# Performance work log

Hardware: AMD Instinct MI355X
Metric: run time of the kernel (lower is better)

Reference implementation:

```python
import jax, jax.numpy as jnp
import numpy as np

TEMPERATURE = 0.5
EPS = 1e-8  # matches F.cosine_similarity eps clamp


def setup_inputs() -> dict:
    key = jax.random.key(0)
    k1, k2 = jax.random.split(key)
    logits = jax.random.normal(k1, (8192, 256), dtype=jnp.float32)
    label = jax.random.randint(k2, (8192,), 0, 10, dtype=jnp.int64)
    return {"logits": logits, "label": label}


def reference(logits, label):
    n = label.shape[0]
    # pairwise cosine similarity via normalize + GEMM (same math as the
    # broadcasted F.cosine_similarity, without the O(n^2 d) intermediate)
    norms = jnp.maximum(jnp.linalg.norm(logits, axis=1, keepdims=True), EPS)
    xn = logits / norms                       # [n, d]
    sim_matrix = xn @ xn.T                    # [n, n]

    eye = jnp.eye(n, dtype=sim_matrix.dtype)
    mask = (label[:, None] == label[None, :]).astype(sim_matrix.dtype)  # same-label (incl. diag)

    e = jnp.exp(sim_matrix / TEMPERATURE) * (1.0 - eye)  # zero diagonal
    sim = mask * e                            # same-label positives
    no_sim_sum = jnp.sum(e - sim, axis=1)     # [n] row sums of different-label terms
    sim_sum = sim + no_sim_sum[:, None]       # denominator per entry
    ratio = sim / sim_sum

    # zeros (different-label entries) get +1 via (1 - mask), diagonal gets +1 via eye -> -log(1) = 0
    loss_mat = -jnp.log((1.0 - mask) + ratio + eye)
    return jnp.sum(loss_mat) / (2 * n)
```

## Files before the change

### kernel.cpp

```cpp
#include <hip/hip_runtime.h>
#include <cstdint>
#include <cstddef>

typedef __bf16 bf16x8 __attribute__((ext_vector_type(8)));
typedef float  f32x4  __attribute__((ext_vector_type(4)));
typedef long long i64;
typedef unsigned char uchar;

#define N_ROWS 8192
#define KDIM   256
#define TEMP_INV 2.0f
#define LOG2E  1.4426950408889634f
#define EXPC   (TEMP_INV * LOG2E)

__device__ __forceinline__ ushort f2bf(float x) {
    uint32_t u = __float_as_uint(x);
    u += 0x7fffu + ((u >> 16) & 1u);
    return (ushort)(u >> 16);
}

__global__ __launch_bounds__(1024) void build_perm(const int* __restrict__ label,
        int* __restrict__ perm, int* __restrict__ labelPerm,
        int* __restrict__ classStart, int* __restrict__ cumTiles)
{
    __shared__ unsigned short lcnt[1024][10];
    __shared__ int cstart[11];
    __shared__ int ccount[10];
    const int tid = threadIdx.x;
    const int wave = tid >> 6, lane = tid & 63;

    int lab[8];
    #pragma unroll
    for (int j = 0; j < 8; ++j) {
        int c = label[tid + j * 1024];
        lab[j] = (c < 0) ? 0 : (c > 9 ? 9 : c);
    }
    unsigned short loc[10] = {0,0,0,0,0,0,0,0,0,0};
    #pragma unroll
    for (int j = 0; j < 8; ++j) loc[lab[j]]++;
    #pragma unroll
    for (int c = 0; c < 10; ++c) lcnt[tid][c] = loc[c];
    __syncthreads();

    if (wave < 10) {
        const int c = wave;
        int s[16]; int tot = 0;
        #pragma unroll
        for (int m = 0; m < 16; ++m) { s[m] = lcnt[lane * 16 + m][c]; tot += s[m]; }
        int incl = tot;
        #pragma unroll
        for (int d = 1; d < 64; d <<= 1) {
            int up = __shfl_up(incl, d, 64);
            if (lane >= d) incl += up;
        }
        int run = incl - tot;
        #pragma unroll
        for (int m = 0; m < 16; ++m) { lcnt[lane * 16 + m][c] = (unsigned short)run; run += s[m]; }
        if (lane == 63) ccount[c] = incl;
    }
    __syncthreads();

    if (tid == 0) {
        int run = 0, runT = 0;
        for (int c = 0; c < 10; ++c) {
            cstart[c] = run; classStart[c] = run;
            int tpc = (ccount[c] + 127) >> 7;
            cumTiles[c] = runT;
            run  += ccount[c];
            runT += tpc * tpc;
        }
        cstart[10] = run; classStart[10] = run; cumTiles[10] = runT;
    }
    __syncthreads();

    int ofs[10];
    #pragma unroll
    for (int c = 0; c < 10; ++c) ofs[c] = lcnt[tid][c];
    #pragma unroll
    for (int j = 0; j < 8; ++j) {
        int c = lab[j];
        int pos = cstart[c] + ofs[c]++;
        perm[pos] = tid + j * 1024;
        labelPerm[pos] = c;
    }
}

__global__ __launch_bounds__(256) void normalize_rows(const float* __restrict__ logits,
        const int* __restrict__ perm, ushort* __restrict__ xn, uchar* __restrict__ xn8)
{
    const int p = blockIdx.x * 4 + (threadIdx.x >> 6);
    const int lane = threadIdx.x & 63;
    const int old = perm[p];
    float4 v = reinterpret_cast<const float4*>(logits + (size_t)old * KDIM)[lane];
    float ss = v.x*v.x + v.y*v.y + v.z*v.z + v.w*v.w;
    #pragma unroll
    for (int off = 32; off >= 1; off >>= 1) ss += __shfl_xor(ss, off, 64);
    float inv = 1.0f / fmaxf(sqrtf(ss), 1e-8f);
    float x0 = v.x * inv, x1 = v.y * inv, x2 = v.z * inv, x3 = v.w * inv;
    ushort4 o;
    o.x = f2bf(x0); o.y = f2bf(x1); o.z = f2bf(x2); o.w = f2bf(x3);
    reinterpret_cast<ushort4*>(xn + (size_t)p * KDIM)[lane] = o;
    int pk = __builtin_amdgcn_cvt_pk_fp8_f32(x0, x1, 0, false);
    pk     = __builtin_amdgcn_cvt_pk_fp8_f32(x2, x3, pk, true);
    reinterpret_cast<unsigned int*>(xn8 + (size_t)p * KDIM)[lane] = (unsigned int)pk;
}

__device__ __forceinline__ void stage_pair_fp8(const uchar* __restrict__ xn8,
        int rowBase, int colBase, int kb, uchar* As, uchar* Bs, int wave, int lane)
{
    #pragma unroll
    for (int it = 0; it < 2; ++it) {
        int ci = it * 256 + wave * 64 + lane;
        int row = ci >> 2;
        int c = (ci & 3) ^ (row & 3);
        const uchar* gA = xn8 + (size_t)(rowBase + row) * KDIM + kb + c * 16;
        const uchar* gB = xn8 + (size_t)(colBase + row) * KDIM + kb + c * 16;
        uchar* lA = As + (size_t)ci * 16;
        uchar* lB = Bs + (size_t)ci * 16;
        __builtin_amdgcn_global_load_lds((const __attribute__((address_space(1))) void*)gA,
                                         (__attribute__((address_space(3))) void*)lA, 16, 0, 0);
        __builtin_amdgcn_global_load_lds((const __attribute__((address_space(1))) void*)gB,
                                         (__attribute__((address_space(3))) void*)lB, 16, 0, 0);
    }
}

__device__ __forceinline__ void read_frags8(const uchar* As, const uchar* Bs,
        i64 (&a)[2][4], i64 (&b)[2][4], int wave, int lane)
{
    const int wr = wave >> 1, wc = wave & 1;
    const int lrow = lane & 15, kgrp = lane >> 4;
    const int ch = kgrp >> 1, half = kgrp & 1;
    #pragma unroll
    for (int kk = 0; kk < 2; ++kk) {
        const int c16 = kk * 2 + ch;
        #pragma unroll
        for (int mi = 0; mi < 4; ++mi) {
            const int row = wr*64 + mi*16 + lrow;
            a[kk][mi] = *reinterpret_cast<const i64*>(As + (size_t)row * 64 + ((c16 ^ (row & 3)) * 16) + half * 8);
        }
        #pragma unroll
        for (int ni = 0; ni < 4; ++ni) {
            const int row = wc*64 + ni*16 + lrow;
            b[kk][ni] = *reinterpret_cast<const i64*>(Bs + (size_t)row * 64 + ((c16 ^ (row & 3)) * 16) + half * 8);
        }
    }
}

__device__ __forceinline__ void mfma_frags8(i64 (&a)[2][4], i64 (&b)[2][4], f32x4 (&acc)[4][4])
{
    #pragma unroll
    for (int kk = 0; kk < 2; ++kk)
        #pragma unroll
        for (int mi = 0; mi < 4; ++mi)
            #pragma unroll
            for (int ni = 0; ni < 4; ++ni)
                acc[mi][ni] = __builtin_amdgcn_mfma_f32_16x16x32_fp8_fp8(a[kk][mi], b[kk][ni], acc[mi][ni], 0, 0, 0);
}

#define PIPE8_READS_RELEASE(Ac, Bc)                                  \
    i64 a[2][4], b[2][4];                                            \
    read_frags8(Ac, Bc, a, b, wave, lane);                           \
    __builtin_amdgcn_sched_barrier(0);                               \
    asm volatile("s_waitcnt lgkmcnt(0)" ::: "memory");               \
    __builtin_amdgcn_sched_barrier(0);                               \
    __builtin_amdgcn_s_barrier();                                    \
    __builtin_amdgcn_sched_barrier(0);

#define PIPE8_MFMA()                                                 \
    __builtin_amdgcn_s_setprio(1);                                   \
    mfma_frags8(a, b, acc);                                          \
    __builtin_amdgcn_s_setprio(0);

#define PIPE8_TAIL(N)                                                \
    __builtin_amdgcn_sched_barrier(0);                               \
    asm volatile("s_waitcnt vmcnt(" #N ")" ::: "memory");            \
    __builtin_amdgcn_s_barrier();                                    \
    __builtin_amdgcn_sched_barrier(0);

__device__ __forceinline__ void kloop_fp8(const uchar* __restrict__ xn8,
        int rowBase, int colBase, f32x4 (&acc)[4][4],
        uchar* As0, uchar* Bs0, uchar* As1, uchar* Bs1, int wave, int lane)
{
    stage_pair_fp8(xn8, rowBase, colBase, 0,  As0, Bs0, wave, lane);
    stage_pair_fp8(xn8, rowBase, colBase, 64, As1, Bs1, wave, lane);
    asm volatile("s_waitcnt vmcnt(4)" ::: "memory");
    __builtin_amdgcn_s_barrier();
    __builtin_amdgcn_sched_barrier(0);
    {
        PIPE8_READS_RELEASE(As0, Bs0)
        stage_pair_fp8(xn8, rowBase, colBase, 128, As0, Bs0, wave, lane);
        PIPE8_MFMA()
        PIPE8_TAIL(4)
    }
    {
        PIPE8_READS_RELEASE(As1, Bs1)
        stage_pair_fp8(xn8, rowBase, colBase, 192, As1, Bs1, wave, lane);
        PIPE8_MFMA()
        PIPE8_TAIL(4)
    }
    {
        PIPE8_READS_RELEASE(As0, Bs0)
        PIPE8_MFMA()
        PIPE8_TAIL(0)
    }
    {
        PIPE8_READS_RELEASE(As1, Bs1)
        PIPE8_MFMA()
    }
}

__global__ __launch_bounds__(256, 4) void phase1_gemm(const uchar* __restrict__ xn8,
        const int* __restrict__ labelPerm, float* __restrict__ pD)
{
    __shared__ __align__(16) char pool[32768];
    uchar* As0 = (uchar*)(pool);
    uchar* Bs0 = (uchar*)(pool + 8192);
    uchar* As1 = (uchar*)(pool + 16384);
    uchar* Bs1 = (uchar*)(pool + 24576);
    float* rowD = (float*)pool;
    float* colD = (float*)(pool + 16384);
    __shared__ int labLDS[256];

    const int tid = threadIdx.x;
    const int wave = tid >> 6, lane = tid & 63;

    int t = blockIdx.x, bi = 0;
    while (t >= 64 - bi) { t -= 64 - bi; ++bi; }
    const int bj = bi + t;
    const bool isDiag = (bi == bj);
    const int rowBase = bi * 128, colBase = bj * 128;

    labLDS[tid] = labelPerm[(tid < 128) ? (rowBase + tid) : (colBase + tid - 128)];
    __builtin_amdgcn_sched_barrier(0);

    f32x4 acc[4][4] = {};
    kloop_fp8(xn8, rowBase, colBase, acc, As0, Bs0, As1, Bs1, wave, lane);

    const int wr = wave >> 1, wc = wave & 1;
    const int lrow = lane & 15, lgrp = lane >> 4;
    float colAcc[4] = {0.f, 0.f, 0.f, 0.f};
    #pragma unroll
    for (int mi = 0; mi < 4; ++mi) {
        #pragma unroll
        for (int reg = 0; reg < 4; ++reg) {
            const int tr = wr * 64 + mi * 16 + lgrp * 4 + reg;
            const int rl = labLDS[tr];
            float rowAcc = 0.f;
            #pragma unroll
            for (int ni = 0; ni < 4; ++ni) {
                const int tc = wc * 64 + ni * 16 + lrow;
                float e = __builtin_amdgcn_exp2f(acc[mi][ni][reg] * EXPC);
                float ed = (rl != labLDS[128 + tc]) ? e : 0.f;
                rowAcc += ed;
                colAcc[ni] += ed;
            }
            rowD[tr * 32 + wc * 16 + lrow] = rowAcc;
        }
    }
    if (!isDiag) {
        #pragma unroll
        for (int ni = 0; ni < 4; ++ni) {
            const int tc = wc * 64 + ni * 16 + lrow;
            colD[tc * 8 + wr * 4 + lgrp] = colAcc[ni];
        }
    }
    __syncthreads();

    if (tid < 128) {
        const float* p = rowD + tid * 32;
        float s = 0.f;
        #pragma unroll
        for (int k = 0; k < 8; ++k) {
            f32x4 v = *reinterpret_cast<const f32x4*>(p + k * 4);
            s += v[0] + v[1] + v[2] + v[3];
        }
        pD[(size_t)bj * N_ROWS + rowBase + tid] = s;
    } else if (!isDiag) {
        const int c2 = tid - 128;
        const float* p = colD + c2 * 8;
        f32x4 v0 = *reinterpret_cast<const f32x4*>(p);
        f32x4 v1 = *reinterpret_cast<const f32x4*>(p + 4);
        pD[(size_t)bi * N_ROWS + colBase + c2] =
            v0[0] + v0[1] + v0[2] + v0[3] + v1[0] + v1[1] + v1[2] + v1[3];
    }
}

__device__ __forceinline__ void stage_tiles(const ushort* __restrict__ xn,
        int rowBase, int colBase, int kb, ushort* As, ushort* Bs, int wave, int lane)
{
    #pragma unroll
    for (int it = 0; it < 4; ++it) {
        int ci = it * 256 + wave * 64 + lane;
        int row = ci >> 3;
        int c = (ci & 7) ^ (row & 7);
        const ushort* gA = xn + (size_t)(rowBase + row) * KDIM + kb + c * 8;
        const ushort* gB = xn + (size_t)(colBase + row) * KDIM + kb + c * 8;
        ushort* lA = As + (size_t)(it * 256 + wave * 64) * 8;
        ushort* lB = Bs + (size_t)(it * 256 + wave * 64) * 8;
        __builtin_amdgcn_global_load_lds((const __attribute__((address_space(1))) void*)gA,
                                         (__attribute__((address_space(3))) void*)lA, 16, 0, 0);
        __builtin_amdgcn_global_load_lds((const __attribute__((address_space(1))) void*)gB,
                                         (__attribute__((address_space(3))) void*)lB, 16, 0, 0);
    }
}

__device__ __forceinline__ void read_frags(const ushort* As, const ushort* Bs,
        bf16x8 (&a)[2][4], bf16x8 (&b)[2][4], int wave, int lane)
{
    const int wr = wave >> 1, wc = wave & 1;
    const int lrow = lane & 15, kgrp = lane >> 4;
    #pragma unroll
    for (int kk = 0; kk < 2; ++kk) {
        const int c = kk * 4 + kgrp;
        #pragma unroll
        for (int mi = 0; mi < 4; ++mi) {
            const int row = wr*64 + mi*16 + lrow;
            a[kk][mi] = *reinterpret_cast<const bf16x8*>(As + (size_t)row * 64 + ((c ^ (row & 7)) * 8));
        }
        #pragma unroll
        for (int ni = 0; ni < 4; ++ni) {
            const int row = wc*64 + ni*16 + lrow;
            b[kk][ni] = *reinterpret_cast<const bf16x8*>(Bs + (size_t)row * 64 + ((c ^ (row & 7)) * 8));
        }
    }
}

__device__ __forceinline__ void mfma_frags(bf16x8 (&a)[2][4], bf16x8 (&b)[2][4],
                                           f32x4 (&acc)[4][4])
{
    #pragma unroll
    for (int kk = 0; kk < 2; ++kk)
        #pragma unroll
        for (int mi = 0; mi < 4; ++mi)
            #pragma unroll
            for (int ni = 0; ni < 4; ++ni)
                acc[mi][ni] = __builtin_amdgcn_mfma_f32_16x16x32_bf16(a[kk][mi], b[kk][ni], acc[mi][ni], 0, 0, 0);
}

#define PIPE_READS_RELEASE(Ac, Bc)                                   \
    bf16x8 a[2][4], b[2][4];                                         \
    read_frags(Ac, Bc, a, b, wave, lane);                            \
    __builtin_amdgcn_sched_barrier(0);                               \
    asm volatile("s_waitcnt lgkmcnt(0)" ::: "memory");               \
    __builtin_amdgcn_sched_barrier(0);                               \
    __builtin_amdgcn_s_barrier();                                    \
    __builtin_amdgcn_sched_barrier(0);

#define PIPE_MFMA()                                                  \
    __builtin_amdgcn_s_setprio(1);                                   \
    mfma_frags(a, b, acc);                                           \
    __builtin_amdgcn_s_setprio(0);

#define PIPE_TAIL(N)                                                 \
    __builtin_amdgcn_sched_barrier(0);                               \
    asm volatile("s_waitcnt vmcnt(" #N ")" ::: "memory");            \
    __builtin_amdgcn_s_barrier();                                    \
    __builtin_amdgcn_sched_barrier(0);

__device__ __forceinline__ void kloop_pipe(const ushort* __restrict__ xn,
        int rowBase, int colBase, f32x4 (&acc)[4][4],
        ushort* As0, ushort* Bs0, ushort* As1, ushort* Bs1, int wave, int lane)
{
    stage_tiles(xn, rowBase, colBase, 0,  As0, Bs0, wave, lane);
    stage_tiles(xn, rowBase, colBase, 64, As1, Bs1, wave, lane);
    asm volatile("s_waitcnt vmcnt(8)" ::: "memory");
    __builtin_amdgcn_s_barrier();
    __builtin_amdgcn_sched_barrier(0);
    {
        PIPE_READS_RELEASE(As0, Bs0)
        stage_tiles(xn, rowBase, colBase, 128, As0, Bs0, wave, lane);
        PIPE_MFMA()
        PIPE_TAIL(8)
    }
    {
        PIPE_READS_RELEASE(As1, Bs1)
        stage_tiles(xn, rowBase, colBase, 192, As1, Bs1, wave, lane);
        PIPE_MFMA()
        PIPE_TAIL(8)
    }
    {
        PIPE_READS_RELEASE(As0, Bs0)
        PIPE_MFMA()
        PIPE_TAIL(0)
    }
    {
        PIPE_READS_RELEASE(As1, Bs1)
        PIPE_MFMA()
    }
}

__global__ __launch_bounds__(256) void phase3_loss(const ushort* __restrict__ xn,
        const float* __restrict__ pD, const int* __restrict__ classStart,
        const int* __restrict__ cumTiles, float* __restrict__ partial)
{
    __shared__ __align__(16) char pool[65536];
    ushort* As0 = (ushort*)(pool);
    ushort* Bs0 = (ushort*)(pool + 16384);
    ushort* As1 = (ushort*)(pool + 32768);
    ushort* Bs1 = (ushort*)(pool + 49152);
    __shared__ float redF[256];
    __shared__ float DarrH[256];
    __shared__ float DarrL[128];
    __shared__ int   meta[22];

    const int tid = threadIdx.x;
    const int wave = tid >> 6, lane = tid & 63;
    const int b = blockIdx.x;

    if (tid < 11) { meta[tid] = classStart[tid]; meta[11 + tid] = cumTiles[tid]; }
    __syncthreads();
    const int nTiles = meta[11 + 10];
    if (b >= nTiles) return;

    int c = 0;
    while (c < 9 && b >= meta[11 + c + 1]) ++c;
    const int s = meta[c], e = meta[c + 1];
    const int nc = e - s;
    const int tps = (nc + 127) >> 7;
    const int lt = b - meta[11 + c];
    const int ti = lt / tps, tj = lt - ti * tps;
    const int rowBase = s + ti * 128, colBase = s + tj * 128;

    {
        const int r = rowBase + (tid & 127);
        const int half = tid >> 7;
        float d = 0.f;
        #pragma unroll 4
        for (int sl = half * 32; sl < half * 32 + 32; ++sl)
            d += pD[(size_t)sl * N_ROWS + r];
        DarrH[(tid & 127) * 2 + half] = d;
    }
    __syncthreads();
    if (tid < 128) DarrL[tid] = DarrH[tid * 2] + DarrH[tid * 2 + 1];
    asm volatile("s_waitcnt vmcnt(0)" ::: "memory");
    __syncthreads();

    f32x4 acc[4][4] = {};
    kloop_pipe(xn, rowBase, colBase, acc, As0, Bs0, As1, Bs1, wave, lane);

    const int wr = wave >> 1, wc = wave & 1;
    const int lrow = lane & 15, lgrp = lane >> 4;
    float lsum = 0.f;
    #pragma unroll
    for (int mi = 0; mi < 4; ++mi) {
        #pragma unroll
        for (int reg = 0; reg < 4; ++reg) {
            const int tr = wr * 64 + mi * 16 + lgrp * 4 + reg;
            const int r = rowBase + tr;
            if (r < e) {
                const float Dr = DarrL[tr];
                #pragma unroll
                for (int ni = 0; ni < 4; ++ni) {
                    const int cg = colBase + wc * 64 + ni * 16 + lrow;
                    if (cg < e && cg != r) {
                        float sim = acc[mi][ni][reg];
                        float ev = __builtin_amdgcn_exp2f(sim * EXPC);
                        lsum += __logf(ev + Dr) - TEMP_INV * sim;
                    }
                }
            }
        }
    }
    redF[tid] = lsum;
    __syncthreads();
    for (int st = 128; st > 0; st >>= 1) {
        if (tid < st) redF[tid] += redF[tid + st];
        __syncthreads();
    }
    if (tid == 0) partial[b] = redF[0];
}

__global__ void phase4_final(const float* __restrict__ partial, const int* __restrict__ cumTiles,
                             float* __restrict__ out)
{
    __shared__ float red[256];
    const int tid = threadIdx.x;
    const int nTiles = cumTiles[10];
    float s = 0.f;
    for (int i = tid; i < nTiles; i += 256) s += partial[i];
    red[tid] = s;
    __syncthreads();
    for (int st = 128; st > 0; st >>= 1) {
        if (tid < st) red[tid] += red[tid + st];
        __syncthreads();
    }
    if (tid == 0) out[0] = red[0] * (1.0f / 16384.0f);
}

extern "C" void kernel_launch(void* const* d_in, const int* in_sizes, int n_in,
                              void* d_out, int out_size, void* d_ws, size_t ws_size,
                              hipStream_t stream)
{
    const float* logits = (const float*)d_in[0];
    const int*   label  = (const int*)d_in[1];
    float* out = (float*)d_out;

    char* ws = (char*)d_ws;
    ushort* xn        = (ushort*)(ws);
    uchar*  xn8       = (uchar*)(ws + (4u << 20));
    float*  pD        = (float*)(ws + (6u << 20));
    int*    perm      = (int*)(ws + (8u << 20));
    int*    labelPerm = (int*)(ws + (8u << 20) + (32u << 10));
    int*    classStart= (int*)(ws + (8u << 20) + (64u << 10));
    int*    cumTiles  = (int*)(ws + (8u << 20) + (64u << 10) + 256);
    float*  partial   = (float*)(ws + (8u << 20) + (128u << 10));

    hipLaunchKernelGGL(build_perm, dim3(1), dim3(1024), 0, stream,
                       label, perm, labelPerm, classStart, cumTiles);
    hipLaunchKernelGGL(normalize_rows, dim3(2048), dim3(256), 0, stream,
                       logits, perm, xn, xn8);
    hipLaunchKernelGGL(phase1_gemm, dim3(2080), dim3(256), 0, stream,
                       xn8, labelPerm, pD);
    hipLaunchKernelGGL(phase3_loss, dim3(4096), dim3(256), 0, stream,
                       xn, pD, classStart, cumTiles, partial);
    hipLaunchKernelGGL(phase4_final, dim3(1), dim3(256), 0, stream,
                       partial, cumTiles, out);
}
```

Before: 70.77 us.

## Exploit symmetry in same-label loss tiles, switch loss GEMM to fp8, skip uniform-label tiles

The per-class loss phase now visits only upper-triangular tiles. Each off-diagonal tile contributes both the row and the column terms, which needs a second D-array load per tile. The loss GEMM moves from bf16 to the same fp8 path as phase 1, so the bf16 normalized copy and its pipeline code are removed. Phase 1 skips tiles whose rows and columns all share one label by writing zero partial sums. Together these cut GEMM work and memory traffic, at the cost of lower precision in the same-label similarities that enter the loss directly, and extra logs per element.

```diff
diff --git a/kernel.cpp b/kernel.cpp
--- a/kernel.cpp
+++ b/kernel.cpp
@@ -2,7 +2,6 @@
 #include <cstdint>
 #include <cstddef>
 
-typedef __bf16 bf16x8 __attribute__((ext_vector_type(8)));
 typedef float  f32x4  __attribute__((ext_vector_type(4)));
 typedef long long i64;
 typedef unsigned char uchar;
@@ -12,12 +11,6 @@
 #define TEMP_INV 2.0f
 #define LOG2E  1.4426950408889634f
 #define EXPC   (TEMP_INV * LOG2E)
-
-__device__ __forceinline__ ushort f2bf(float x) {
-    uint32_t u = __float_as_uint(x);
-    u += 0x7fffu + ((u >> 16) & 1u);
-    return (ushort)(u >> 16);
-}
 
 __global__ __launch_bounds__(1024) void build_perm(const int* __restrict__ label,
         int* __restrict__ perm, int* __restrict__ labelPerm,
@@ -67,7 +60,7 @@
             int tpc = (ccount[c] + 127) >> 7;
             cumTiles[c] = runT;
             run  += ccount[c];
-            runT += tpc * tpc;
+            runT += tpc * (tpc + 1) / 2;
         }
         cstart[10] = run; classStart[10] = run; cumTiles[10] = runT;
     }
@@ -86,7 +79,7 @@
 }
 
 __global__ __launch_bounds__(256) void normalize_rows(const float* __restrict__ logits,
-        const int* __restrict__ perm, ushort* __restrict__ xn, uchar* __restrict__ xn8)
+        const int* __restrict__ perm, uchar* __restrict__ xn8)
 {
     const int p = blockIdx.x * 4 + (threadIdx.x >> 6);
     const int lane = threadIdx.x & 63;
@@ -97,9 +90,6 @@
     for (int off = 32; off >= 1; off >>= 1) ss += __shfl_xor(ss, off, 64);
     float inv = 1.0f / fmaxf(sqrtf(ss), 1e-8f);
     float x0 = v.x * inv, x1 = v.y * inv, x2 = v.z * inv, x3 = v.w * inv;
-    ushort4 o;
-    o.x = f2bf(x0); o.y = f2bf(x1); o.z = f2bf(x2); o.w = f2bf(x3);
-    reinterpret_cast<ushort4*>(xn + (size_t)p * KDIM)[lane] = o;
     int pk = __builtin_amdgcn_cvt_pk_fp8_f32(x0, x1, 0, false);
     pk     = __builtin_amdgcn_cvt_pk_fp8_f32(x2, x3, pk, true);
     reinterpret_cast<unsigned int*>(xn8 + (size_t)p * KDIM)[lane] = (unsigned int)pk;
@@ -229,6 +219,12 @@
     const int bj = bi + t;
     const bool isDiag = (bi == bj);
     const int rowBase = bi * 128, colBase = bj * 128;
+
+    if (labelPerm[rowBase] == labelPerm[colBase + 127]) {
+        if (tid < 128)       pD[(size_t)bj * N_ROWS + rowBase + tid] = 0.f;
+        else if (!isDiag)    pD[(size_t)bi * N_ROWS + colBase + tid - 128] = 0.f;
+        return;
+    }
 
     labLDS[tid] = labelPerm[(tid < 128) ? (rowBase + tid) : (colBase + tid - 128)];
     __builtin_amdgcn_sched_barrier(0);
@@ -285,122 +281,19 @@
     }
 }
 
-__device__ __forceinline__ void stage_tiles(const ushort* __restrict__ xn,
-        int rowBase, int colBase, int kb, ushort* As, ushort* Bs, int wave, int lane)
-{
-    #pragma unroll
-    for (int it = 0; it < 4; ++it) {
-        int ci = it * 256 + wave * 64 + lane;
-        int row = ci >> 3;
-        int c = (ci & 7) ^ (row & 7);
-        const ushort* gA = xn + (size_t)(rowBase + row) * KDIM + kb + c * 8;
-        const ushort* gB = xn + (size_t)(colBase + row) * KDIM + kb + c * 8;
-        ushort* lA = As + (size_t)(it * 256 + wave * 64) * 8;
-        ushort* lB = Bs + (size_t)(it * 256 + wave * 64) * 8;
-        __builtin_amdgcn_global_load_lds((const __attribute__((address_space(1))) void*)gA,
-                                         (__attribute__((address_space(3))) void*)lA, 16, 0, 0);
-        __builtin_amdgcn_global_load_lds((const __attribute__((address_space(1))) void*)gB,
-                                         (__attribute__((address_space(3))) void*)lB, 16, 0, 0);
-    }
-}
-
-__device__ __forceinline__ void read_frags(const ushort* As, const ushort* Bs,
-        bf16x8 (&a)[2][4], bf16x8 (&b)[2][4], int wave, int lane)
-{
-    const int wr = wave >> 1, wc = wave & 1;
-    const int lrow = lane & 15, kgrp = lane >> 4;
-    #pragma unroll
-    for (int kk = 0; kk < 2; ++kk) {
-        const int c = kk * 4 + kgrp;
-        #pragma unroll
-        for (int mi = 0; mi < 4; ++mi) {
-            const int row = wr*64 + mi*16 + lrow;
-            a[kk][mi] = *reinterpret_cast<const bf16x8*>(As + (size_t)row * 64 + ((c ^ (row & 7)) * 8));
-        }
-        #pragma unroll
-        for (int ni = 0; ni < 4; ++ni) {
-            const int row = wc*64 + ni*16 + lrow;
-            b[kk][ni] = *reinterpret_cast<const bf16x8*>(Bs + (size_t)row * 64 + ((c ^ (row & 7)) * 8));
-        }
-    }
-}
-
-__device__ __forceinline__ void mfma_frags(bf16x8 (&a)[2][4], bf16x8 (&b)[2][4],
-                                           f32x4 (&acc)[4][4])
-{
-    #pragma unroll
-    for (int kk = 0; kk < 2; ++kk)
-        #pragma unroll
-        for (int mi = 0; mi < 4; ++mi)
-            #pragma unroll
-            for (int ni = 0; ni < 4; ++ni)
-                acc[mi][ni] = __builtin_amdgcn_mfma_f32_16x16x32_bf16(a[kk][mi], b[kk][ni], acc[mi][ni], 0, 0, 0);
-}
-
-#define PIPE_READS_RELEASE(Ac, Bc)                                   \
-    bf16x8 a[2][4], b[2][4];                                         \
-    read_frags(Ac, Bc, a, b, wave, lane);                            \
-    __builtin_amdgcn_sched_barrier(0);                               \
-    asm volatile("s_waitcnt lgkmcnt(0)" ::: "memory");               \
-    __builtin_amdgcn_sched_barrier(0);                               \
-    __builtin_amdgcn_s_barrier();                                    \
-    __builtin_amdgcn_sched_barrier(0);
-
-#define PIPE_MFMA()                                                  \
-    __builtin_amdgcn_s_setprio(1);                                   \
-    mfma_frags(a, b, acc);                                           \
-    __builtin_amdgcn_s_setprio(0);
-
-#define PIPE_TAIL(N)                                                 \
-    __builtin_amdgcn_sched_barrier(0);                               \
-    asm volatile("s_waitcnt vmcnt(" #N ")" ::: "memory");            \
-    __builtin_amdgcn_s_barrier();                                    \
-    __builtin_amdgcn_sched_barrier(0);
-
-__device__ __forceinline__ void kloop_pipe(const ushort* __restrict__ xn,
-        int rowBase, int colBase, f32x4 (&acc)[4][4],
-        ushort* As0, ushort* Bs0, ushort* As1, ushort* Bs1, int wave, int lane)
-{
-    stage_tiles(xn, rowBase, colBase, 0,  As0, Bs0, wave, lane);
-    stage_tiles(xn, rowBase, colBase, 64, As1, Bs1, wave, lane);
-    asm volatile("s_waitcnt vmcnt(8)" ::: "memory");
-    __builtin_amdgcn_s_barrier();
-    __builtin_amdgcn_sched_barrier(0);
-    {
-        PIPE_READS_RELEASE(As0, Bs0)
-        stage_tiles(xn, rowBase, colBase, 128, As0, Bs0, wave, lane);
-        PIPE_MFMA()
-        PIPE_TAIL(8)
-    }
-    {
-        PIPE_READS_RELEASE(As1, Bs1)
-        stage_tiles(xn, rowBase, colBase, 192, As1, Bs1, wave, lane);
-        PIPE_MFMA()
-        PIPE_TAIL(8)
-    }
-    {
-        PIPE_READS_RELEASE(As0, Bs0)
-        PIPE_MFMA()
-        PIPE_TAIL(0)
-    }
-    {
-        PIPE_READS_RELEASE(As1, Bs1)
-        PIPE_MFMA()
-    }
-}
-
-__global__ __launch_bounds__(256) void phase3_loss(const ushort* __restrict__ xn,
+__global__ __launch_bounds__(256, 4) void phase3_loss(const uchar* __restrict__ xn8,
         const float* __restrict__ pD, const int* __restrict__ classStart,
         const int* __restrict__ cumTiles, float* __restrict__ partial)
 {
-    __shared__ __align__(16) char pool[65536];
-    ushort* As0 = (ushort*)(pool);
-    ushort* Bs0 = (ushort*)(pool + 16384);
-    ushort* As1 = (ushort*)(pool + 32768);
-    ushort* Bs1 = (ushort*)(pool + 49152);
+    __shared__ __align__(16) char pool[32768];
+    uchar* As0 = (uchar*)(pool);
+    uchar* Bs0 = (uchar*)(pool + 8192);
+    uchar* As1 = (uchar*)(pool + 16384);
+    uchar* Bs1 = (uchar*)(pool + 24576);
     __shared__ float redF[256];
     __shared__ float DarrH[256];
-    __shared__ float DarrL[128];
+    __shared__ float DarrR[128];
+    __shared__ float DarrC[128];
     __shared__ int   meta[22];
 
     const int tid = threadIdx.x;
@@ -417,12 +310,15 @@
     const int s = meta[c], e = meta[c + 1];
     const int nc = e - s;
     const int tps = (nc + 127) >> 7;
-    const int lt = b - meta[11 + c];
-    const int ti = lt / tps, tj = lt - ti * tps;
+    int lt = b - meta[11 + c];
+    int ti = 0;
+    while (lt >= tps - ti) { lt -= tps - ti; ++ti; }
+    const int tj = ti + lt;
+    const bool isDiagT = (ti == tj);
     const int rowBase = s + ti * 128, colBase = s + tj * 128;
 
     {
-        const int r = rowBase + (tid & 127);
+        int r = rowBase + (tid & 127); if (r > N_ROWS - 1) r = N_ROWS - 1;
         const int half = tid >> 7;
         float d = 0.f;
         #pragma unroll 4
@@ -431,12 +327,24 @@
         DarrH[(tid & 127) * 2 + half] = d;
     }
     __syncthreads();
-    if (tid < 128) DarrL[tid] = DarrH[tid * 2] + DarrH[tid * 2 + 1];
+    if (tid < 128) DarrR[tid] = DarrH[tid * 2] + DarrH[tid * 2 + 1];
+    __syncthreads();
+    if (!isDiagT) {
+        int r = colBase + (tid & 127); if (r > N_ROWS - 1) r = N_ROWS - 1;
+        const int half = tid >> 7;
+        float d = 0.f;
+        #pragma unroll 4
+        for (int sl = half * 32; sl < half * 32 + 32; ++sl)
+            d += pD[(size_t)sl * N_ROWS + r];
+        DarrH[(tid & 127) * 2 + half] = d;
+        __syncthreads();
+        if (tid < 128) DarrC[tid] = DarrH[tid * 2] + DarrH[tid * 2 + 1];
+    }
     asm volatile("s_waitcnt vmcnt(0)" ::: "memory");
     __syncthreads();
 
     f32x4 acc[4][4] = {};
-    kloop_pipe(xn, rowBase, colBase, acc, As0, Bs0, As1, Bs1, wave, lane);
+    kloop_fp8(xn8, rowBase, colBase, acc, As0, Bs0, As1, Bs1, wave, lane);
 
     const int wr = wave >> 1, wc = wave & 1;
     const int lrow = lane & 15, lgrp = lane >> 4;
@@ -448,14 +356,21 @@
             const int tr = wr * 64 + mi * 16 + lgrp * 4 + reg;
             const int r = rowBase + tr;
             if (r < e) {
-                const float Dr = DarrL[tr];
+                const float Dr = DarrR[tr];
                 #pragma unroll
                 for (int ni = 0; ni < 4; ++ni) {
-                    const int cg = colBase + wc * 64 + ni * 16 + lrow;
-                    if (cg < e && cg != r) {
+                    const int tc = wc * 64 + ni * 16 + lrow;
+                    const int cg = colBase + tc;
+                    if (cg < e) {
                         float sim = acc[mi][ni][reg];
                         float ev = __builtin_amdgcn_exp2f(sim * EXPC);
-                        lsum += __logf(ev + Dr) - TEMP_INV * sim;
+                        if (isDiagT) {
+                            if (cg != r)
+                                lsum += __logf(ev + Dr) - TEMP_INV * sim;
+                        } else {
+                            lsum += __logf(ev + Dr) + __logf(ev + DarrC[tc])
+                                  - 2.0f * TEMP_INV * sim;
+                        }
                     }
                 }
             }
@@ -496,23 +411,22 @@
     float* out = (float*)d_out;
 
     char* ws = (char*)d_ws;
-    ushort* xn        = (ushort*)(ws);
-    uchar*  xn8       = (uchar*)(ws + (4u << 20));
-    float*  pD        = (float*)(ws + (6u << 20));
-    int*    perm      = (int*)(ws + (8u << 20));
-    int*    labelPerm = (int*)(ws + (8u << 20) + (32u << 10));
-    int*    classStart= (int*)(ws + (8u << 20) + (64u << 10));
-    int*    cumTiles  = (int*)(ws + (8u << 20) + (64u << 10) + 256);
-    float*  partial   = (float*)(ws + (8u << 20) + (128u << 10));
+    uchar*  xn8       = (uchar*)(ws);
+    float*  pD        = (float*)(ws + (2u << 20));
+    int*    perm      = (int*)(ws + (4u << 20));
+    int*    labelPerm = (int*)(ws + (4u << 20) + (32u << 10));
+    int*    classStart= (int*)(ws + (4u << 20) + (64u << 10));
+    int*    cumTiles  = (int*)(ws + (4u << 20) + (64u << 10) + 256);
+    float*  partial   = (float*)(ws + (4u << 20) + (128u << 10));
 
     hipLaunchKernelGGL(build_perm, dim3(1), dim3(1024), 0, stream,
                        label, perm, labelPerm, classStart, cumTiles);
     hipLaunchKernelGGL(normalize_rows, dim3(2048), dim3(256), 0, stream,
-                       logits, perm, xn, xn8);
+                       logits, perm, xn8);
     hipLaunchKernelGGL(phase1_gemm, dim3(2080), dim3(256), 0, stream,
                        xn8, labelPerm, pD);
-    hipLaunchKernelGGL(phase3_loss, dim3(4096), dim3(256), 0, stream,
-                       xn, pD, classStart, cumTiles, partial);
+    hipLaunchKernelGGL(phase3_loss, dim3(2080), dim3(256), 0, stream,
+                       xn8, pD, classStart, cumTiles, partial);
     hipLaunchKernelGGL(phase4_final, dim3(1), dim3(256), 0, stream,
                        partial, cumTiles, out);
 }
```

Result: slower. 73.09 us (+3.3%).
